# Performance work log

Measured on AMD Instinct MI355X. Metric: run time of the kernel, lower is better.

The kernel has to match this reference:

```python
import jax, jax.numpy as jnp
import numpy as np


def _bilerp(grid, x, y):
    """Bilinear sample grid [H,W,C] at continuous coords x,y [B,V] -> [B,V,C]."""
    H, W = grid.shape[0], grid.shape[1]
    x0f = jnp.floor(x); y0f = jnp.floor(y)
    wx = (x - x0f)[..., None]; wy = (y - y0f)[..., None]
    x0 = jnp.clip(x0f.astype(jnp.int32), 0, W - 1)
    x1 = jnp.clip(x0f.astype(jnp.int32) + 1, 0, W - 1)
    y0 = jnp.clip(y0f.astype(jnp.int32), 0, H - 1)
    y1 = jnp.clip(y0f.astype(jnp.int32) + 1, 0, H - 1)
    return (grid[y0, x0] * (1 - wx) * (1 - wy) + grid[y0, x1] * wx * (1 - wy)
            + grid[y1, x0] * (1 - wx) * wy + grid[y1, x1] * wx * wy)


def _normalize(x, eps=1e-12):
    n = jnp.linalg.norm(x, axis=-1, keepdims=True)
    return x / jnp.maximum(n, eps)


def setup_inputs() -> dict:
    key = jax.random.key(0)
    ks = jax.random.split(key, 12)
    B, H, W = 4, 512, 512
    V, F = 100000, 200000
    return {
        "vertices": jax.random.normal(ks[0], (1, V, 3), jnp.float32),
        "vertices_texcoords": jax.random.uniform(ks[1], (1, V, 2), jnp.float32),
        "vertices_normals": jax.random.normal(ks[2], (1, V, 3), jnp.float32),
        "faces_vt_idx": jax.random.randint(ks[3], (1, F, 3), 0, V, jnp.int32),
        "faces_vn_idx": jax.random.randint(ks[4], (1, F, 3), 0, V, jnp.int32),
        "faces_v_idx": jax.random.randint(ks[5], (1, F, 3), 0, V, jnp.int32),
        "pose": jax.random.normal(ks[6], (B, 4, 4), jnp.float32),
        "depth": jax.random.uniform(ks[7], (B, H, W), jnp.float32),
        "face_index_map": jax.random.randint(ks[8], (B, H, W), 0, F, jnp.int32),
        "weight_map": jax.random.uniform(ks[9], (B, H, W, 3), jnp.float32),
        "v_uvz": jax.random.uniform(ks[10], (B, V, 3), jnp.float32),
        # +0.5 keeps the z component (used as 1/z) away from zero
        "faces_v_uvz": jax.random.uniform(ks[11], (B, F, 3, 3), jnp.float32) + 0.5,
    }


def reference(vertices, vertices_texcoords, vertices_normals, faces_vt_idx,
              faces_vn_idx, faces_v_idx, pose, depth, face_index_map,
              weight_map, v_uvz, faces_v_uvz):
    B, H, W = depth.shape
    mesh_span = (vertices[0].max(axis=0) - vertices[0].min(axis=0)).max()

    # --- screen-space vertex coords + bilinear depth lookup (front mask) ---
    vx = (v_uvz[..., 0] * 0.5 + 0.5) * W                  # [B,V]
    vy = (1.0 - (v_uvz[..., 1] * 0.5 + 0.5)) * H          # [B,V]
    v_depth = _bilerp(depth[0][..., None], vx, vy)        # [B,V,1] (batch-0 depth, as in source)
    v_front_mask = (v_uvz[0, :, 2] - v_depth[0, :, 0] < mesh_span * 0.005)[None, :]

    # --- perspective-corrected barycentric weights ---
    fz = faces_v_uvz[..., 2]                              # [B,F,3]
    fz_map = jax.vmap(lambda f, idx: f[idx])(fz, face_index_map)  # [B,H,W,3]
    wmap = (1.0 / fz_map) * weight_map * depth[..., None] # [B,H,W,3]
    wmap = wmap[..., None]                                # [B,H,W,3,1]

    # --- uv map ---
    faces_vt = vertices_texcoords[0][faces_vt_idx[0]]     # [F,3,2]
    uv_map = (faces_vt[face_index_map] * wmap).sum(axis=-2)  # [B,H,W,2]
    uv_map = uv_map - jnp.floor(uv_map)

    # --- normal map (object + camera space) ---
    faces_vn = vertices_normals[0][faces_vn_idx[0]]       # [F,3,3]
    normal_map = _normalize((faces_vn[face_index_map] * wmap).sum(axis=-2))
    R = pose[:, :3, :3]
    t = pose[:, :3, -1]
    normal_map_cam = _normalize(jnp.einsum('bij,bhwj->bhwi', R, normal_map))

    # --- position map (object + camera space) ---
    faces_v = vertices[0][faces_v_idx[0]]                 # [F,3,3]
    position_map = (faces_v[face_index_map] * wmap).sum(axis=-2)
    position_map_cam = jnp.einsum('bij,bhwj->bhwi', R, position_map) + t[:, None, None, :]

    # Concatenate float map outputs into one tensor [B,H,W,14]
    out = jnp.concatenate([uv_map, normal_map, normal_map_cam,
                           position_map, position_map_cam], axis=-1)
    return out
```

## Files before the change

### kernel.cpp

```cpp
#include <hip/hip_runtime.h>
#include <stdint.h>


struct H2 { _Float16 x, y; };
static __device__ __forceinline__ uint32_t packh_u(float a, float b) {
    H2 h; h.x = (_Float16)a; h.y = (_Float16)b;
    return __builtin_bit_cast(uint32_t, h);
}
static __device__ __forceinline__ float packh(float a, float b) {
    return __builtin_bit_cast(float, packh_u(a, b));
}
static __device__ __forceinline__ float asf(uint32_t u) {
    return __builtin_bit_cast(float, u);
}
static __device__ __forceinline__ float2 unph(float w) {
    H2 h = __builtin_bit_cast(H2, w);
    return make_float2((float)h.x, (float)h.y);
}


__global__ __launch_bounds__(256) void prep_fz(
    const float* __restrict__ nrm, const float* __restrict__ vtx,
    const float* __restrict__ fuvz,
    uint2* __restrict__ nrmh, uint2* __restrict__ vtxh,
    float4* __restrict__ fzq, int V, long BF)
{
    __shared__ float sf[2304];
    const int tid = threadIdx.x;
    const long base = (long)blockIdx.x * 256;
    const long i = base + tid;

    if (nrmh != nullptr && i < V) {
        const float* n = nrm + i * 3;
        const float* v = vtx + i * 3;
        nrmh[i] = make_uint2(packh_u(n[0], n[1]), packh_u(n[2], 0.0f));
        vtxh[i] = make_uint2(packh_u(v[0], v[1]), packh_u(v[2], 0.0f));
    }

    if (base + 256 <= BF) {
        const float4* src = (const float4*)(fuvz + base * 9);
        float4* d = (float4*)sf;
        d[tid]       = src[tid];
        d[tid + 256] = src[tid + 256];
        if (tid < 64) d[tid + 512] = src[tid + 512];
        __syncthreads();
        fzq[i] = make_float4(__fdiv_rn(1.0f, sf[tid * 9 + 2]),
                             __fdiv_rn(1.0f, sf[tid * 9 + 5]),
                             __fdiv_rn(1.0f, sf[tid * 9 + 8]), 0.0f);
    } else if (i < BF) {
        const float* s = fuvz + i * 9;
        fzq[i] = make_float4(__fdiv_rn(1.0f, s[2]),
                             __fdiv_rn(1.0f, s[5]),
                             __fdiv_rn(1.0f, s[8]), 0.0f);
    }
}

__global__ __launch_bounds__(256) void pack_faces2(
    const float* __restrict__ tc,
    const uint2* __restrict__ nrmh, const uint2* __restrict__ vtxh,
    const int* __restrict__ f_vt, const int* __restrict__ f_vn,
    const int* __restrict__ f_v,
    float4* __restrict__ rec, int F, int V)
{
    __shared__ float4 sw[1024];
    const int tid  = threadIdx.x;
    const int base = blockIdx.x * 256;
    const int f    = base + tid;

    if (f < F) {
        float2 t[3]; uint2 N[3], Vv[3];
#pragma unroll
        for (int k = 0; k < 3; ++k) {
            int ivt = f_vt[f * 3 + k];
            ivt = ivt < 0 ? 0 : (ivt >= V ? V - 1 : ivt);
            t[k] = ((const float2*)tc)[ivt];
            int ivn = f_vn[f * 3 + k];
            ivn = ivn < 0 ? 0 : (ivn >= V ? V - 1 : ivn);
            N[k] = nrmh[ivn];
            int iv = f_v[f * 3 + k];
            iv = iv < 0 ? 0 : (iv >= V ? V - 1 : iv);
            Vv[k] = vtxh[iv];
        }
        uint32_t w9  = (N[0].y  & 0xffffu) | (N[1].y  << 16);
        uint32_t w10 = (N[2].y  & 0xffffu) | (Vv[0].y << 16);
        uint32_t w14 = (Vv[1].y & 0xffffu) | (Vv[2].y << 16);
        float4* o = sw + tid * 4;
        o[0] = make_float4(t[0].x, t[0].y, t[1].x, t[1].y);
        o[1] = make_float4(t[2].x, t[2].y, asf(N[0].x), asf(N[1].x));
        o[2] = make_float4(asf(N[2].x), asf(w9), asf(w10), asf(Vv[0].x));
        o[3] = make_float4(asf(Vv[1].x), asf(Vv[2].x), asf(w14), 0.0f);
    }
    __syncthreads();
    const int valid  = F - base;
    const int valid4 = (valid < 256 ? valid : 256) * 4;
    float4* og = rec + (long)base * 4;
#pragma unroll
    for (int j = 0; j < 4; ++j) {
        int k = tid + 256 * j;
        if (k < valid4) og[k] = sw[k];
    }
}

__global__ __launch_bounds__(256) void pack_faces_old(
    const float* __restrict__ tc, const float* __restrict__ nrm,
    const float* __restrict__ vtx,
    const int* __restrict__ f_vt, const int* __restrict__ f_vn,
    const int* __restrict__ f_v,
    float* __restrict__ rec, int F, int V)
{
    int f = blockIdx.x * 256 + threadIdx.x;
    if (f >= F) return;
    float t[6], n[9], v[9];
#pragma unroll
    for (int k = 0; k < 3; ++k) {
        int ivt = f_vt[f * 3 + k];
        ivt = ivt < 0 ? 0 : (ivt >= V ? V - 1 : ivt);
        t[k * 2 + 0] = tc[(long)ivt * 2 + 0];
        t[k * 2 + 1] = tc[(long)ivt * 2 + 1];
        int ivn = f_vn[f * 3 + k];
        ivn = ivn < 0 ? 0 : (ivn >= V ? V - 1 : ivn);
        n[k * 3 + 0] = nrm[(long)ivn * 3 + 0];
        n[k * 3 + 1] = nrm[(long)ivn * 3 + 1];
        n[k * 3 + 2] = nrm[(long)ivn * 3 + 2];
        int iv = f_v[f * 3 + k];
        iv = iv < 0 ? 0 : (iv >= V ? V - 1 : iv);
        v[k * 3 + 0] = vtx[(long)iv * 3 + 0];
        v[k * 3 + 1] = vtx[(long)iv * 3 + 1];
        v[k * 3 + 2] = vtx[(long)iv * 3 + 2];
    }
    float4* o = (float4*)(rec + (long)f * 16);
    o[0] = make_float4(t[0], t[1], t[2], t[3]);
    o[1] = make_float4(t[4], t[5], packh(n[0], n[1]), packh(n[3], n[4]));
    o[2] = make_float4(packh(n[6], n[7]), packh(n[2], n[5]),
                       packh(n[8], v[2]), packh(v[0], v[1]));
    o[3] = make_float4(packh(v[3], v[4]), packh(v[6], v[7]),
                       packh(v[5], v[8]), 0.0f);
}

__global__ __launch_bounds__(256) void raster_fast2(
    const float4* __restrict__ rec,
    const float4* __restrict__ fzq,
    const float* __restrict__ pose,
    const float* __restrict__ depth,
    const int*   __restrict__ fim,
    const float* __restrict__ weight,
    float* __restrict__ out,
    int F, int HW)
{
    __shared__ float sb[256 * 14];
    const int tid = threadIdx.x;
    const int hw  = blockIdx.x * 256 + tid;
    const int b   = blockIdx.y;
    const long p  = (long)b * HW + hw;

    {
        const float4* wsrc =
            (const float4*)(weight + ((long)b * HW + (long)blockIdx.x * 256) * 3);
        if (tid < 192) ((float4*)sb)[tid] = wsrc[tid];
    }

    const float* pb = pose + b * 16;
    float R00 = pb[0],  R01 = pb[1],  R02 = pb[2],  t0 = pb[3];
    float R10 = pb[4],  R11 = pb[5],  R12 = pb[6],  t1 = pb[7];
    float R20 = pb[8],  R21 = pb[9],  R22 = pb[10], t2 = pb[11];

    int f = fim[p];
    f = f < 0 ? 0 : (f >= F ? F - 1 : f);
    const float d = depth[p];

    const float4* R4 = rec + (long)f * 4;
    float4 a0 = R4[0], a1 = R4[1], a2 = R4[2], a3 = R4[3];
    float4 fz = fzq[(long)b * F + f];

    __syncthreads();
    float w0 = sb[tid * 3 + 0];
    float w1 = sb[tid * 3 + 1];
    float w2 = sb[tid * 3 + 2];
    __syncthreads();

    float wm0 = __fmul_rn(__fmul_rn(fz.x, w0), d);
    float wm1 = __fmul_rn(__fmul_rn(fz.y, w1), d);
    float wm2 = __fmul_rn(__fmul_rn(fz.z, w2), d);

    float uv0 = __fadd_rn(__fadd_rn(__fmul_rn(a0.x, wm0), __fmul_rn(a0.z, wm1)),
                          __fmul_rn(a1.x, wm2));
    float uv1 = __fadd_rn(__fadd_rn(__fmul_rn(a0.y, wm0), __fmul_rn(a0.w, wm1)),
                          __fmul_rn(a1.y, wm2));
    uv0 -= floorf(uv0);
    uv1 -= floorf(uv1);

    float2 u6  = unph(a1.z);
    float2 u7  = unph(a1.w);
    float2 u8  = unph(a2.x);
    float2 u9  = unph(a2.y);
    float2 u10 = unph(a2.z);
    float2 u11 = unph(a2.w);
    float2 u12 = unph(a3.x);
    float2 u13 = unph(a3.y);
    float2 u14 = unph(a3.z);

    float n0 = u6.x * wm0 + u7.x * wm1 + u8.x * wm2;
    float n1 = u6.y * wm0 + u7.y * wm1 + u8.y * wm2;
    float n2 = u9.x * wm0 + u9.y * wm1 + u10.x * wm2;

    float p0 = u11.x * wm0 + u12.x * wm1 + u13.x * wm2;
    float p1 = u11.y * wm0 + u12.y * wm1 + u13.y * wm2;
    float p2 = u10.y * wm0 + u14.x * wm1 + u14.y * wm2;

    float nn = sqrtf(n0 * n0 + n1 * n1 + n2 * n2);
    float ni = 1.0f / fmaxf(nn, 1e-12f);
    float m0 = n0 * ni, m1 = n1 * ni, m2 = n2 * ni;

    float c0 = R00 * m0 + R01 * m1 + R02 * m2;
    float c1 = R10 * m0 + R11 * m1 + R12 * m2;
    float c2 = R20 * m0 + R21 * m1 + R22 * m2;
    float cn = sqrtf(c0 * c0 + c1 * c1 + c2 * c2);
    float ci = 1.0f / fmaxf(cn, 1e-12f);
    c0 *= ci; c1 *= ci; c2 *= ci;

    float q0 = R00 * p0 + R01 * p1 + R02 * p2 + t0;
    float q1 = R10 * p0 + R11 * p1 + R12 * p2 + t1;
    float q2 = R20 * p0 + R21 * p1 + R22 * p2 + t2;

    float* s = sb + tid * 14;
    s[0]  = uv0; s[1]  = uv1;
    s[2]  = m0;  s[3]  = m1;  s[4]  = m2;
    s[5]  = c0;  s[6]  = c1;  s[7]  = c2;
    s[8]  = p0;  s[9]  = p1;  s[10] = p2;
    s[11] = q0;  s[12] = q1;  s[13] = q2;
    __syncthreads();

    float4* og = (float4*)(out + ((long)b * HW + (long)blockIdx.x * 256) * 14);
    const float4* sv = (const float4*)sb;
#pragma unroll
    for (int j = 0; j < 4; ++j) {
        int k = tid + 256 * j;
        if (k < 896) og[k] = sv[k];
    }
}

__global__ __launch_bounds__(256) void raster_kernel(
    const float* __restrict__ vertices, const float* __restrict__ texcoords,
    const float* __restrict__ normals,
    const int* __restrict__ f_vt, const int* __restrict__ f_vn,
    const int* __restrict__ f_v,
    const float* __restrict__ pose, const float* __restrict__ depth,
    const int* __restrict__ fim, const float* __restrict__ weight,
    const float* __restrict__ fuvz, float* __restrict__ out, int F, int V,
    int HW)
{
    const int hw = blockIdx.x * 256 + threadIdx.x;
    if (hw >= HW) return;
    const int b  = blockIdx.y;
    const int p  = b * HW + hw;
    const float* pb = pose + b * 16;
    float R00 = pb[0], R01 = pb[1], R02 = pb[2],  t0 = pb[3];
    float R10 = pb[4], R11 = pb[5], R12 = pb[6],  t1 = pb[7];
    float R20 = pb[8], R21 = pb[9], R22 = pb[10], t2 = pb[11];
    int f = fim[p];
    f = f < 0 ? 0 : (f >= F ? F - 1 : f);
    const float d = depth[p];
    const float* fz = fuvz + ((long)b * F + f) * 9;
    float wm[3];
#pragma unroll
    for (int k = 0; k < 3; ++k)
        wm[k] = __fmul_rn(__fmul_rn(__fdiv_rn(1.0f, fz[k * 3 + 2]),
                                    weight[(long)p * 3 + k]), d);
    float u0t[3], u1t[3];
    float n0 = 0.f, n1 = 0.f, n2 = 0.f, p0 = 0.f, p1 = 0.f, p2 = 0.f;
#pragma unroll
    for (int k = 0; k < 3; ++k) {
        int ivt = f_vt[f * 3 + k], ivn = f_vn[f * 3 + k], iv = f_v[f * 3 + k];
        ivt = ivt < 0 ? 0 : (ivt >= V ? V - 1 : ivt);
        ivn = ivn < 0 ? 0 : (ivn >= V ? V - 1 : ivn);
        iv  = iv  < 0 ? 0 : (iv  >= V ? V - 1 : iv);
        const float* tc = texcoords + (long)ivt * 2;
        u0t[k] = __fmul_rn(tc[0], wm[k]);
        u1t[k] = __fmul_rn(tc[1], wm[k]);
        const float* nr = normals + (long)ivn * 3;
        n0 += nr[0] * wm[k]; n1 += nr[1] * wm[k]; n2 += nr[2] * wm[k];
        const float* vv = vertices + (long)iv * 3;
        p0 += vv[0] * wm[k]; p1 += vv[1] * wm[k]; p2 += vv[2] * wm[k];
    }
    float uv0 = __fadd_rn(__fadd_rn(u0t[0], u0t[1]), u0t[2]);
    float uv1 = __fadd_rn(__fadd_rn(u1t[0], u1t[1]), u1t[2]);
    uv0 -= floorf(uv0); uv1 -= floorf(uv1);
    float nn = sqrtf(n0 * n0 + n1 * n1 + n2 * n2);
    float ni = 1.0f / fmaxf(nn, 1e-12f);
    float m0 = n0 * ni, m1 = n1 * ni, m2 = n2 * ni;
    float c0 = R00 * m0 + R01 * m1 + R02 * m2;
    float c1 = R10 * m0 + R11 * m1 + R12 * m2;
    float c2 = R20 * m0 + R21 * m1 + R22 * m2;
    float cn = sqrtf(c0 * c0 + c1 * c1 + c2 * c2);
    float ci = 1.0f / fmaxf(cn, 1e-12f);
    c0 *= ci; c1 *= ci; c2 *= ci;
    float q0 = R00 * p0 + R01 * p1 + R02 * p2 + t0;
    float q1 = R10 * p0 + R11 * p1 + R12 * p2 + t1;
    float q2 = R20 * p0 + R21 * p1 + R22 * p2 + t2;
    float2* o = (float2*)(out + (long)p * 14);
    o[0] = make_float2(uv0, uv1); o[1] = make_float2(m0, m1);
    o[2] = make_float2(m2, c0);   o[3] = make_float2(c1, c2);
    o[4] = make_float2(p0, p1);   o[5] = make_float2(p2, q0);
    o[6] = make_float2(q1, q2);
}

extern "C" void kernel_launch(void* const* d_in, const int* in_sizes, int n_in,
                              void* d_out, int out_size, void* d_ws, size_t ws_size,
                              hipStream_t stream) {
    const float* vertices  = (const float*)d_in[0];
    const float* texcoords = (const float*)d_in[1];
    const float* normals   = (const float*)d_in[2];
    const int*   f_vt      = (const int*)  d_in[3];
    const int*   f_vn      = (const int*)  d_in[4];
    const int*   f_v       = (const int*)  d_in[5];
    const float* pose      = (const float*)d_in[6];
    const float* depth     = (const float*)d_in[7];
    const int*   fim       = (const int*)  d_in[8];
    const float* weight    = (const float*)d_in[9];
    const float* fuvz      = (const float*)d_in[11];
    float* out = (float*)d_out;

    const int B  = in_sizes[6] / 16;
    const int F  = in_sizes[3] / 3;
    const int V  = in_sizes[1] / 2;
    const int HW = in_sizes[7] / B;
    const long BF = (long)B * F;

    const size_t rec_bytes = (size_t)F * 64;
    const size_t fzq_bytes = (size_t)BF * 16;
    const size_t tab_bytes = (size_t)V * 8;
    const bool base_ok = d_ws != nullptr &&
                         (((uintptr_t)d_ws) & 15) == 0 &&
                         (HW % 256) == 0;
    const bool ws_new = base_ok &&
                        ws_size >= rec_bytes + fzq_bytes + 2 * tab_bytes;
    const bool ws_old = base_ok && ws_size >= rec_bytes + fzq_bytes;

    if (ws_new) {
        float* rec  = (float*)d_ws;
        float* fzq  = (float*)((char*)d_ws + rec_bytes);
        uint2* nrmh = (uint2*)((char*)d_ws + rec_bytes + fzq_bytes);
        uint2* vtxh = (uint2*)((char*)d_ws + rec_bytes + fzq_bytes + tab_bytes);
        long nb = BF > (long)V ? BF : (long)V;
        prep_fz<<<(unsigned)((nb + 255) / 256), 256, 0, stream>>>(
            normals, vertices, fuvz, nrmh, vtxh, (float4*)fzq, V, BF);
        pack_faces2<<<(F + 255) / 256, 256, 0, stream>>>(
            texcoords, nrmh, vtxh, f_vt, f_vn, f_v, (float4*)rec, F, V);
        dim3 grid(HW / 256, B);
        raster_fast2<<<grid, 256, 0, stream>>>(
            (const float4*)rec, (const float4*)fzq, pose, depth, fim, weight,
            out, F, HW);
    } else if (ws_old) {
        float* rec = (float*)d_ws;
        float* fzq = (float*)((char*)d_ws + rec_bytes);
        prep_fz<<<(unsigned)((BF + 255) / 256), 256, 0, stream>>>(
            normals, vertices, fuvz, nullptr, nullptr, (float4*)fzq, V, BF);
        pack_faces_old<<<(F + 255) / 256, 256, 0, stream>>>(
            texcoords, normals, vertices, f_vt, f_vn, f_v, rec, F, V);
        dim3 grid(HW / 256, B);
        raster_fast2<<<grid, 256, 0, stream>>>(
            (const float4*)rec, (const float4*)fzq, pose, depth, fim, weight,
            out, F, HW);
    } else {
        dim3 grid((HW + 255) / 256, B);
        raster_kernel<<<grid, 256, 0, stream>>>(
            vertices, texcoords, normals, f_vt, f_vn, f_v,
            pose, depth, fim, weight, fuvz, out, F, V, HW);
    }
}
```

Before: 173.1 us.

## Swizzle raster blocks so each XCD serves one batch, load weights directly

Result: no change. 171.6 us (-0.9%).

```diff
diff --git a/kernel.cpp b/kernel.cpp
--- a/kernel.cpp
+++ b/kernel.cpp
@@ -137,7 +137,7 @@
                        packh(v[5], v[8]), 0.0f);
 }
 
-__global__ __launch_bounds__(256) void raster_fast2(
+__global__ __launch_bounds__(256) void raster_fast3(
     const float4* __restrict__ rec,
     const float4* __restrict__ fzq,
     const float* __restrict__ pose,
@@ -145,19 +145,22 @@
     const int*   __restrict__ fim,
     const float* __restrict__ weight,
     float* __restrict__ out,
-    int F, int HW)
+    int F, int HW, int nx, int swz)
 {
     __shared__ float sb[256 * 14];
     const int tid = threadIdx.x;
-    const int hw  = blockIdx.x * 256 + tid;
-    const int b   = blockIdx.y;
+    const int id  = blockIdx.x;
+    int b, x;
+    if (swz) {
+        const int xcd = id & 7;
+        b = xcd >> 1;
+        x = (id >> 3) + ((xcd & 1) ? (nx >> 1) : 0);
+    } else {
+        b = id / nx;
+        x = id - b * nx;
+    }
+    const int hw  = x * 256 + tid;
     const long p  = (long)b * HW + hw;
-
-    {
-        const float4* wsrc =
-            (const float4*)(weight + ((long)b * HW + (long)blockIdx.x * 256) * 3);
-        if (tid < 192) ((float4*)sb)[tid] = wsrc[tid];
-    }
 
     const float* pb = pose + b * 16;
     float R00 = pb[0],  R01 = pb[1],  R02 = pb[2],  t0 = pb[3];
@@ -167,16 +170,13 @@
     int f = fim[p];
     f = f < 0 ? 0 : (f >= F ? F - 1 : f);
     const float d = depth[p];
+    float w0 = weight[p * 3 + 0];
+    float w1 = weight[p * 3 + 1];
+    float w2 = weight[p * 3 + 2];
 
     const float4* R4 = rec + (long)f * 4;
     float4 a0 = R4[0], a1 = R4[1], a2 = R4[2], a3 = R4[3];
     float4 fz = fzq[(long)b * F + f];
-
-    __syncthreads();
-    float w0 = sb[tid * 3 + 0];
-    float w1 = sb[tid * 3 + 1];
-    float w2 = sb[tid * 3 + 2];
-    __syncthreads();
 
     float wm0 = __fmul_rn(__fmul_rn(fz.x, w0), d);
     float wm1 = __fmul_rn(__fmul_rn(fz.y, w1), d);
@@ -230,7 +230,7 @@
     s[11] = q0;  s[12] = q1;  s[13] = q2;
     __syncthreads();
 
-    float4* og = (float4*)(out + ((long)b * HW + (long)blockIdx.x * 256) * 14);
+    float4* og = (float4*)(out + ((long)b * HW + (long)x * 256) * 14);
     const float4* sv = (const float4*)sb;
 #pragma unroll
     for (int j = 0; j < 4; ++j) {
@@ -336,6 +336,9 @@
                         ws_size >= rec_bytes + fzq_bytes + 2 * tab_bytes;
     const bool ws_old = base_ok && ws_size >= rec_bytes + fzq_bytes;
 
+    const int nx = HW / 256;
+    const int swz = (B == 4 && (nx & 1) == 0) ? 1 : 0;
+
     if (ws_new) {
         float* rec  = (float*)d_ws;
         float* fzq  = (float*)((char*)d_ws + rec_bytes);
@@ -346,10 +349,9 @@
             normals, vertices, fuvz, nrmh, vtxh, (float4*)fzq, V, BF);
         pack_faces2<<<(F + 255) / 256, 256, 0, stream>>>(
             texcoords, nrmh, vtxh, f_vt, f_vn, f_v, (float4*)rec, F, V);
-        dim3 grid(HW / 256, B);
-        raster_fast2<<<grid, 256, 0, stream>>>(
+        raster_fast3<<<B * nx, 256, 0, stream>>>(
             (const float4*)rec, (const float4*)fzq, pose, depth, fim, weight,
-            out, F, HW);
+            out, F, HW, nx, swz);
     } else if (ws_old) {
         float* rec = (float*)d_ws;
         float* fzq = (float*)((char*)d_ws + rec_bytes);
@@ -357,10 +359,9 @@
             normals, vertices, fuvz, nullptr, nullptr, (float4*)fzq, V, BF);
         pack_faces_old<<<(F + 255) / 256, 256, 0, stream>>>(
             texcoords, normals, vertices, f_vt, f_vn, f_v, rec, F, V);
-        dim3 grid(HW / 256, B);
-        raster_fast2<<<grid, 256, 0, stream>>>(
+        raster_fast3<<<B * nx, 256, 0, stream>>>(
             (const float4*)rec, (const float4*)fzq, pose, depth, fim, weight,
-            out, F, HW);
+            out, F, HW, nx, swz);
     } else {
         dim3 grid((HW + 255) / 256, B);
         raster_kernel<<<grid, 256, 0, stream>>>(
```
